# Kernel optimization log

Measured on AMD Instinct MI355X. Metric: run time of the kernel, lower is better.

## Reference

```python
import jax, jax.numpy as jnp
import numpy as np

B, S, D = 2, 2048, 1024
H, DH = 16, 64
E, K, FH = 8, 2, 4096
AUX_W = 0.01
EPS = 1e-6


def setup_inputs() -> dict:
    key = jax.random.key(0)
    ks = jax.random.split(key, 20)
    init = lambda k, shape: (jax.random.normal(k, shape, dtype=jnp.float32) * 0.02)
    return {
        'x': jax.random.normal(ks[0], (B, S, D), dtype=jnp.float32),
        'ln1_s': jnp.ones((D,), jnp.float32), 'ln1_b': jnp.zeros((D,), jnp.float32),
        'Wq': init(ks[1], (D, H * DH)), 'bq': jnp.zeros((H * DH,), jnp.float32),
        'Wk': init(ks[2], (D, H * DH)), 'bk': jnp.zeros((H * DH,), jnp.float32),
        'Wv': init(ks[3], (D, H * DH)), 'bv': jnp.zeros((H * DH,), jnp.float32),
        'Wo': init(ks[4], (H * DH, D)), 'bo': jnp.zeros((D,), jnp.float32),
        'ln2_s': jnp.ones((D,), jnp.float32), 'ln2_b': jnp.zeros((D,), jnp.float32),
        'Wg': init(ks[5], (D, E)), 'bg': jnp.zeros((E,), jnp.float32),
        'W1': init(ks[6], (E, D, FH)), 'b1': jnp.zeros((E, FH), jnp.float32),
        'W2': init(ks[7], (E, FH, D)), 'b2': jnp.zeros((E, D), jnp.float32),
    }


def _layer_norm(x, scale, bias):
    mu = jnp.mean(x, axis=-1, keepdims=True)
    var = jnp.mean(jnp.square(x - mu), axis=-1, keepdims=True)
    return (x - mu) * jax.lax.rsqrt(var + EPS) * scale + bias


def _causal_attn(x, Wq, bq, Wk, bk, Wv, bv, Wo, bo):
    b, s, _ = x.shape
    q = (x @ Wq + bq).reshape(b, s, H, DH)
    k = (x @ Wk + bk).reshape(b, s, H, DH)
    v = (x @ Wv + bv).reshape(b, s, H, DH)
    scores = jnp.einsum('bqhd,bkhd->bhqk', q, k) / jnp.sqrt(jnp.float32(DH))
    causal = jnp.tril(jnp.ones((s, s), dtype=bool))
    scores = jnp.where(causal, scores, jnp.finfo(scores.dtype).min)
    attn = jax.nn.softmax(scores, axis=-1)
    out = jnp.einsum('bhqk,bkhd->bqhd', attn, v).reshape(b, s, H * DH)
    return out @ Wo + bo


def _moe(x, Wg, bg, W1, b1, W2, b2):
    # x: (B,S,D) -> tokens (T,D)
    T = x.shape[0] * x.shape[1]
    xf = x.reshape(T, D)
    logits = xf @ Wg + bg                      # (T,E)
    probs = jax.nn.softmax(logits, axis=-1)
    topv, topi = jax.lax.top_k(probs, K)       # (T,K)
    topv = topv / jnp.sum(topv, axis=-1, keepdims=True)
    combine = jnp.zeros((T, E), xf.dtype).at[jnp.arange(T)[:, None], topi].set(topv)
    out = jnp.zeros((T, D), xf.dtype)
    for e in range(E):  # fixed small expert loop
        h = jax.nn.gelu(xf @ W1[e] + b1[e])
        out = out + combine[:, e:e + 1] * (h @ W2[e] + b2[e])
    # load-balance aux loss
    frac = jnp.mean((combine > 0).astype(jnp.float32), axis=0)
    pmean = jnp.mean(probs, axis=0)
    aux = AUX_W * E * jnp.sum(frac * pmean)
    return out.reshape(x.shape), aux


def reference(x, ln1_s, ln1_b, Wq, bq, Wk, bk, Wv, bv, Wo, bo,
              ln2_s, ln2_b, Wg, bg, W1, b1, W2, b2):
    working = x
    attn_in = _layer_norm(working, ln1_s, ln1_b)
    attn_out = _causal_attn(attn_in, Wq, bq, Wk, bk, Wv, bv, Wo, bo)
    working = working + attn_out
    ffn_in = _layer_norm(working, ln2_s, ln2_b)
    ffn_out, aux = _moe(ffn_in, Wg, bg, W1, b1, W2, b2)
    output = working + ffn_out
    return output, aux
```

## Files before the change

kernel.cpp:

```cpp
#include <hip/hip_runtime.h>
#include <hip/hip_bf16.h>
#include <math.h>

#define Bb 2
#define Ss 2048
#define Dd 1024
#define Hh 16
#define DH 64
#define Ee 8
#define FH 4096
#define Tt (Bb*Ss)

typedef __attribute__((ext_vector_type(8))) short short8;
typedef __attribute__((ext_vector_type(4))) short short4v;
typedef __attribute__((ext_vector_type(4))) float float4v;

static __device__ inline short f2bf(float f) {
    __hip_bfloat16 h = __float2bfloat16(f);
    return *reinterpret_cast<short*>(&h);
}

static __device__ inline void glds16(const __hip_bfloat16* g, __hip_bfloat16* l) {
    __builtin_amdgcn_global_load_lds(
        (const __attribute__((address_space(1))) unsigned int*)g,
        (__attribute__((address_space(3))) unsigned int*)l, 16, 0, 0);
}

__global__ __launch_bounds__(256) void ln_kernel(const float* __restrict__ x,
                                                 const float* __restrict__ sc,
                                                 const float* __restrict__ bi,
                                                 __hip_bfloat16* __restrict__ y) {
    int t = blockIdx.x, tid = threadIdx.x;
    const float* xr = x + (size_t)t * Dd;
    float s1 = 0.f, s2 = 0.f;
    for (int d = tid; d < Dd; d += 256) { float v = xr[d]; s1 += v; s2 += v * v; }
    __shared__ float r1[256], r2[256];
    r1[tid] = s1; r2[tid] = s2; __syncthreads();
    for (int off = 128; off > 0; off >>= 1) {
        if (tid < off) { r1[tid] += r1[tid + off]; r2[tid] += r2[tid + off]; }
        __syncthreads();
    }
    float mu = r1[0] * (1.f / Dd);
    float var = r2[0] * (1.f / Dd) - mu * mu;
    float rstd = rsqrtf(var + 1e-6f);
    __hip_bfloat16* yr = y + (size_t)t * Dd;
    for (int d = tid; d < Dd; d += 256) {
        float v = xr[d];
        yr[d] = __float2bfloat16((v - mu) * rstd * sc[d] + bi[d]);
    }
}

__global__ __launch_bounds__(256) void transpose_qkvo(
    const float* W0, const float* W1, const float* W2, const float* W3,
    __hip_bfloat16* T0, __hip_bfloat16* T1, __hip_bfloat16* T2, __hip_bfloat16* T3) {
    int z = blockIdx.z;
    const float* W = (z == 0) ? W0 : (z == 1) ? W1 : (z == 2) ? W2 : W3;
    __hip_bfloat16* Wt = (z == 0) ? T0 : (z == 1) ? T1 : (z == 2) ? T2 : T3;
    __shared__ float tile[64][65];
    int k0 = blockIdx.y * 64, n0 = blockIdx.x * 64;
    int tx = threadIdx.x & 15, ty = threadIdx.x >> 4;
    #pragma unroll
    for (int p = 0; p < 4; p++) {
        float4 v = *(const float4*)(&W[(size_t)(k0 + ty + p * 16) * Dd + n0 + tx * 4]);
        tile[ty + p * 16][tx * 4 + 0] = v.x;
        tile[ty + p * 16][tx * 4 + 1] = v.y;
        tile[ty + p * 16][tx * 4 + 2] = v.z;
        tile[ty + p * 16][tx * 4 + 3] = v.w;
    }
    __syncthreads();
    #pragma unroll
    for (int p = 0; p < 4; p++) {
        int n = ty + p * 16;
        short4v pk;
        pk[0] = f2bf(tile[tx * 4 + 0][n]);
        pk[1] = f2bf(tile[tx * 4 + 1][n]);
        pk[2] = f2bf(tile[tx * 4 + 2][n]);
        pk[3] = f2bf(tile[tx * 4 + 3][n]);
        *(short4v*)(&Wt[(size_t)(n0 + n) * Dd + k0 + tx * 4]) = pk;
    }
}

__global__ __launch_bounds__(256) void transpose_we(const float* __restrict__ W,
                                                    __hip_bfloat16* __restrict__ Wt,
                                                    int Kd, int N) {
    int e = blockIdx.z;
    W  += (size_t)e * Kd * N;
    Wt += (size_t)e * Kd * N;
    __shared__ float tile[64][65];
    int k0 = blockIdx.y * 64, n0 = blockIdx.x * 64;
    int tx = threadIdx.x & 15, ty = threadIdx.x >> 4;
    #pragma unroll
    for (int p = 0; p < 4; p++) {
        float4 v = *(const float4*)(&W[(size_t)(k0 + ty + p * 16) * N + n0 + tx * 4]);
        tile[ty + p * 16][tx * 4 + 0] = v.x;
        tile[ty + p * 16][tx * 4 + 1] = v.y;
        tile[ty + p * 16][tx * 4 + 2] = v.z;
        tile[ty + p * 16][tx * 4 + 3] = v.w;
    }
    __syncthreads();
    #pragma unroll
    for (int p = 0; p < 4; p++) {
        int n = ty + p * 16;
        short4v pk;
        pk[0] = f2bf(tile[tx * 4 + 0][n]);
        pk[1] = f2bf(tile[tx * 4 + 1][n]);
        pk[2] = f2bf(tile[tx * 4 + 2][n]);
        pk[3] = f2bf(tile[tx * 4 + 3][n]);
        *(short4v*)(&Wt[(size_t)(n0 + n) * Kd + k0 + tx * 4]) = pk;
    }
}

template<int MODE, int NS = 1>
__global__ __launch_bounds__(256) void gemm_mfma(
    const __hip_bfloat16* __restrict__ A, const __hip_bfloat16* __restrict__ Bt,
    const float* __restrict__ bias, void* __restrict__ Cv,
    int M, int N, int Kd,
    const int* __restrict__ bucket, const int* __restrict__ cnts,
    const int* __restrict__ bases, const float* __restrict__ residual,
    const float* __restrict__ bias_k, const float* __restrict__ bias_v,
    void* __restrict__ Ck, void* __restrict__ Cv2)
{
    int Me = M;
    const int* rowIdx = nullptr;
    int hbase = 0;
    int ksplit = 0;
    int zsel = 0;
    if (MODE == 2 || MODE == 3) {
        int e = (NS == 2) ? (blockIdx.z >> 1) : blockIdx.z;
        if (NS == 2) ksplit = blockIdx.z & 1;
        Me = cnts[e];
        hbase = bases[e];
        Bt += (size_t)e * N * Kd;
        bias += (size_t)e * N;
        if (MODE == 2) rowIdx = bucket + e * Tt;
        if (MODE == 3) A += (size_t)hbase * Kd;
    }
    if (MODE == 5) {
        zsel = blockIdx.z;
        Bt += (size_t)zsel * Dd * Dd;
        if (zsel == 1) bias = bias_k;
        if (zsel == 2) bias = bias_v;
    }
    int m0 = blockIdx.y * 128;
    if (m0 >= Me) return;
    int n0 = blockIdx.x * 128;

    __shared__ __hip_bfloat16 As[2 * 128 * 32];
    __shared__ __hip_bfloat16 Bs[2 * 128 * 32];

    int tid = threadIdx.x;
    int lane = tid & 63, wave = tid >> 6;
    int wm = (wave & 1) * 64, wn = (wave >> 1) * 64;
    int quad = lane >> 4, l16 = lane & 15;

    int rs = lane >> 2;
    int sslot = (lane & 3) ^ ((lane >> 3) & 3);
    int rowS0 = 16 * (2 * wave + 0) + rs;
    int rowS1 = 16 * (2 * wave + 1) + rs;

    const __hip_bfloat16 *gA0, *gA1;
    if (MODE == 2) {
        int g0 = m0 + rowS0, g1 = m0 + rowS1;
        int r0 = (g0 < Me) ? rowIdx[g0] : 0;
        int r1 = (g1 < Me) ? rowIdx[g1] : 0;
        gA0 = A + (size_t)r0 * Kd + sslot * 8;
        gA1 = A + (size_t)r1 * Kd + sslot * 8;
    } else {
        gA0 = A + (size_t)(m0 + rowS0) * Kd + sslot * 8;
        gA1 = A + (size_t)(m0 + rowS1) * Kd + sslot * 8;
    }
    const __hip_bfloat16* gB0 = Bt + (size_t)(n0 + rowS0) * Kd + sslot * 8;
    const __hip_bfloat16* gB1 = Bt + (size_t)(n0 + rowS1) * Kd + sslot * 8;

    __hip_bfloat16* lA0 = As + (2 * wave + 0) * 512;
    __hip_bfloat16* lA1 = As + (2 * wave + 1) * 512;
    __hip_bfloat16* lB0 = Bs + (2 * wave + 0) * 512;
    __hip_bfloat16* lB1 = Bs + (2 * wave + 1) * 512;

    int rsw = (l16 >> 1) & 3;
    int rdoff = (quad ^ rsw) * 8;

    float4v acc[4][4];
    #pragma unroll
    for (int i = 0; i < 4; i++)
        #pragma unroll
        for (int j = 0; j < 4; j++) acc[i][j] = (float4v)0.f;

    const int NT = Kd >> 5;
    int t0s = 0, t1s = NT;
    if (NS == 2) { int hlf = NT >> 1; t0s = ksplit * hlf; t1s = t0s + hlf; }

    {
        int ko = t0s << 5;
        glds16(gA0 + ko, lA0);
        glds16(gA1 + ko, lA1);
        glds16(gB0 + ko, lB0);
        glds16(gB1 + ko, lB1);
    }
    __syncthreads();

    int cur = 0;
    for (int t = t0s; t < t1s; t++) {
        if (t + 1 < t1s) {
            int ko = (t + 1) << 5;
            int bo = (cur ^ 1) * 4096;
            glds16(gA0 + ko, lA0 + bo);
            glds16(gA1 + ko, lA1 + bo);
            glds16(gB0 + ko, lB0 + bo);
            glds16(gB1 + ko, lB1 + bo);
        }
        int cb = cur * 4096;
        short8 af[4], bf[4];
        #pragma unroll
        for (int i = 0; i < 4; i++)
            af[i] = *(const short8*)(&As[cb + (wm + i * 16 + l16) * 32 + rdoff]);
        #pragma unroll
        for (int j = 0; j < 4; j++)
            bf[j] = *(const short8*)(&Bs[cb + (wn + j * 16 + l16) * 32 + rdoff]);
        #pragma unroll
        for (int i = 0; i < 4; i++)
            #pragma unroll
            for (int j = 0; j < 4; j++)
                acc[i][j] = __builtin_amdgcn_mfma_f32_16x16x32_bf16(af[i], bf[j], acc[i][j], 0, 0, 0);
        __syncthreads();
        cur ^= 1;
    }

    #pragma unroll
    for (int i = 0; i < 4; i++) {
        #pragma unroll
        for (int j = 0; j < 4; j++) {
            int col = n0 + wn + j * 16 + l16;
            float bsv = (MODE == 3 && NS == 2 && ksplit == 1) ? 0.f : bias[col];
            if (MODE == 4 || (MODE == 5 && zsel == 2)) {
                __hip_bfloat16* vt = (__hip_bfloat16*)((MODE == 5) ? Cv2 : Cv);
                int mb = m0 + wm + i * 16 + quad * 4;
                int b = mb >> 11, s0 = mb & (Ss - 1);
                int h = col >> 6, d = col & (DH - 1);
                short4v pk;
                #pragma unroll
                for (int r = 0; r < 4; r++) pk[r] = f2bf(acc[i][j][r] + bsv);
                *(short4v*)(vt + ((size_t)(b * Hh + h) * DH + d) * Ss + s0) = pk;
                continue;
            }
            #pragma unroll
            for (int r = 0; r < 4; r++) {
                int m = m0 + wm + i * 16 + quad * 4 + r;
                if (m >= Me) continue;
                float val = acc[i][j][r] + bsv;
                if (MODE == 0) {
                    ((__hip_bfloat16*)Cv)[(size_t)m * N + col] = __float2bfloat16(val);
                } else if (MODE == 5) {
                    __hip_bfloat16* co = (__hip_bfloat16*)((zsel == 0) ? Cv : Ck);
                    co[(size_t)m * N + col] = __float2bfloat16(val);
                } else if (MODE == 1) {
                    ((float*)Cv)[(size_t)m * N + col] = val + residual[(size_t)m * N + col];
                } else if (MODE == 2) {
                    float z = 0.7978845608028654f * (val + 0.044715f * val * val * val);
                    float eg = __expf(2.f * z);
                    float th = 1.f - __fdividef(2.f, eg + 1.f);
                    ((__hip_bfloat16*)Cv)[(size_t)(hbase + m) * N + col] =
                        __float2bfloat16(0.5f * val * (1.f + th));
                } else {
                    float* o3 = (float*)((NS == 2 && ksplit == 1) ? Cv2 : Cv);
                    o3[(size_t)(hbase + m) * N + col] = val;
                }
            }
        }
    }
}

__global__ __launch_bounds__(256) void attn_mfma(const __hip_bfloat16* __restrict__ q,
                                                 const __hip_bfloat16* __restrict__ k,
                                                 const __hip_bfloat16* __restrict__ Vt,
                                                 __hip_bfloat16* __restrict__ out) {
    int h = blockIdx.x, tile = blockIdx.y, b = blockIdx.z;
    int wave = threadIdx.x >> 6, lane = threadIdx.x & 63;
    int quad = lane >> 4, l16 = lane & 15;
    int q0 = tile * 64 + wave * 16;
    int tb = b * Ss;

    __shared__ __hip_bfloat16 Ks[32 * 72];
    __shared__ __hip_bfloat16 Vs[64 * 40];

    const __hip_bfloat16* qp = q + (size_t)(tb + q0 + l16) * (Hh * DH) + h * DH + quad * 8;
    short8 qf0 = *(const short8*)(qp);
    short8 qf1 = *(const short8*)(qp + 32);

    float4v oc[4];
    #pragma unroll
    for (int i = 0; i < 4; i++) oc[i] = (float4v)0.f;
    float lsum = 0.f;

    const __hip_bfloat16* kbase = k + (size_t)tb * (Hh * DH) + h * DH;
    const __hip_bfloat16* vbase = Vt + ((size_t)(b * Hh + h) * DH) * Ss;
    int qglob = q0 + l16;
    int srcA = (quad & 1) * 32 + l16;
    int srcB = srcA + 16;
    int sel = quad >> 1;
    int nsteps = 2 * tile + 2;

    int krow = threadIdx.x >> 3, kg = threadIdx.x & 7;
    int vd   = threadIdx.x >> 2, vg = threadIdx.x & 3;

    short8 kv = *(const short8*)(kbase + (size_t)krow * (Hh * DH) + kg * 8);
    short8 vv = *(const short8*)(vbase + (size_t)vd * Ss + vg * 8);

    for (int st = 0; st < nsteps; st++) {
        int k0 = st * 32;
        *(short8*)(&Ks[krow * 72 + kg * 8]) = kv;
        *(short8*)(&Vs[vd * 40 + vg * 8]) = vv;
        __syncthreads();
        if (st + 1 < nsteps) {
            kv = *(const short8*)(kbase + (size_t)(k0 + 32 + krow) * (Hh * DH) + kg * 8);
            vv = *(const short8*)(vbase + (size_t)vd * Ss + (k0 + 32) + vg * 8);
        }

        short8 a0 = *(const short8*)(&Ks[l16 * 72 + quad * 8]);
        short8 a1 = *(const short8*)(&Ks[l16 * 72 + 32 + quad * 8]);
        short8 a2 = *(const short8*)(&Ks[(l16 + 16) * 72 + quad * 8]);
        short8 a3 = *(const short8*)(&Ks[(l16 + 16) * 72 + 32 + quad * 8]);

        float4v c0 = (float4v)0.f, c1 = (float4v)0.f;
        c0 = __builtin_amdgcn_mfma_f32_16x16x32_bf16(a0, qf0, c0, 0, 0, 0);
        c0 = __builtin_amdgcn_mfma_f32_16x16x32_bf16(a1, qf1, c0, 0, 0, 0);
        c1 = __builtin_amdgcn_mfma_f32_16x16x32_bf16(a2, qf0, c1, 0, 0, 0);
        c1 = __builtin_amdgcn_mfma_f32_16x16x32_bf16(a3, qf1, c1, 0, 0, 0);

        float p0[4], p1[4];
        #pragma unroll
        for (int r = 0; r < 4; r++) {
            int key0 = k0 + quad * 4 + r;
            int key1 = key0 + 16;
            p0[r] = (key0 <= qglob) ? __expf(c0[r] * 0.125f - 4.f) : 0.f;
            p1[r] = (key1 <= qglob) ? __expf(c1[r] * 0.125f - 4.f) : 0.f;
            lsum += p0[r] + p1[r];
        }

        short8 pf;
        #pragma unroll
        for (int r = 0; r < 4; r++) {
            float t0 = __shfl(p0[r], srcA), t1 = __shfl(p1[r], srcA);
            pf[r] = f2bf(sel ? t1 : t0);
            float u0 = __shfl(p0[r], srcB), u1 = __shfl(p1[r], srcB);
            pf[4 + r] = f2bf(sel ? u1 : u0);
        }

        #pragma unroll
        for (int nt = 0; nt < 4; nt++) {
            short8 bv = *(const short8*)(&Vs[(nt * 16 + l16) * 40 + quad * 8]);
            oc[nt] = __builtin_amdgcn_mfma_f32_16x16x32_bf16(pf, bv, oc[nt], 0, 0, 0);
        }
        __syncthreads();
    }

    lsum += __shfl_xor(lsum, 16);
    lsum += __shfl_xor(lsum, 32);
    float linv[4];
    #pragma unroll
    for (int r = 0; r < 4; r++) linv[r] = 1.f / __shfl(lsum, quad * 4 + r);

    #pragma unroll
    for (int nt = 0; nt < 4; nt++) {
        #pragma unroll
        for (int r = 0; r < 4; r++) {
            int tokq = tb + q0 + quad * 4 + r;
            out[(size_t)tokq * (Hh * DH) + h * DH + nt * 16 + l16] =
                __float2bfloat16(oc[nt][r] * linv[r]);
        }
    }
}

#define GT 64
__global__ __launch_bounds__(256) void gate_kernel(const float* __restrict__ wk,
                                                   const float* __restrict__ g2s,
                                                   const float* __restrict__ g2b,
                                                   const float* __restrict__ Wg,
                                                   const float* __restrict__ bg,
                                                   float* __restrict__ psum,
                                                   int* __restrict__ counts,
                                                   int* __restrict__ bucket,
                                                   int* __restrict__ eidx,
                                                   int* __restrict__ epos,
                                                   float* __restrict__ ew) {
    int t0 = blockIdx.x * GT;
    int wave = threadIdx.x >> 6, lane = threadIdx.x & 63;

    __shared__ float sp[GT][Ee];
    __shared__ int   sel_e[2][GT];
    __shared__ int   spos[2][GT];
    __shared__ int   lbase[Ee];

    for (int i = wave; i < GT; i += 4) {
        int t = t0 + i;
        const float* xr = wk + (size_t)t * Dd;
        float xv[16];
        float s1 = 0.f, sq = 0.f;
        #pragma unroll
        for (int j = 0; j < 16; j++) {
            float v = xr[lane + j * 64];
            xv[j] = v; s1 += v; sq += v * v;
        }
        #pragma unroll
        for (int off = 32; off; off >>= 1) { s1 += __shfl_xor(s1, off); sq += __shfl_xor(sq, off); }
        float mu = s1 * (1.f / Dd), var = sq * (1.f / Dd) - mu * mu;
        float rstd = rsqrtf(var + 1e-6f);
        float acc[Ee] = {};
        #pragma unroll
        for (int j = 0; j < 16; j++) {
            int d = lane + j * 64;
            float xn = (xv[j] - mu) * rstd * g2s[d] + g2b[d];
            const float* wr = Wg + d * Ee;
            #pragma unroll
            for (int e = 0; e < Ee; e++) acc[e] += xn * wr[e];
        }
        #pragma unroll
        for (int e = 0; e < Ee; e++)
            #pragma unroll
            for (int off = 32; off; off >>= 1) acc[e] += __shfl_xor(acc[e], off);
        if (lane == 0) {
            float lg[Ee], mx = -1e30f;
            #pragma unroll
            for (int e = 0; e < Ee; e++) { lg[e] = acc[e] + bg[e]; mx = fmaxf(mx, lg[e]); }
            float p[Ee], ssum = 0.f;
            #pragma unroll
            for (int e = 0; e < Ee; e++) { p[e] = __expf(lg[e] - mx); ssum += p[e]; }
            float ise = 1.f / ssum;
            #pragma unroll
            for (int e = 0; e < Ee; e++) { p[e] *= ise; sp[i][e] = p[e]; }
            int e1 = 0;
            for (int e = 1; e < Ee; e++) if (p[e] > p[e1]) e1 = e;
            int e2 = -1;
            for (int e = 0; e < Ee; e++) if (e != e1 && (e2 < 0 || p[e] > p[e2])) e2 = e;
            sel_e[0][i] = e1; sel_e[1][i] = e2;
            float w1 = p[e1], w2 = p[e2], isw = 1.f / (w1 + w2);
            eidx[2 * t] = e1; ew[2 * t] = w1 * isw;
            eidx[2 * t + 1] = e2; ew[2 * t + 1] = w2 * isw;
        }
    }
    __syncthreads();

    if (threadIdx.x < Ee) {
        int e = threadIdx.x;
        int local = 0;
        for (int i = 0; i < GT; i++) {
            if (sel_e[0][i] == e) spos[0][i] = local++;
            if (sel_e[1][i] == e) spos[1][i] = local++;
        }
        lbase[e] = atomicAdd(&counts[e], local);
        float ps = 0.f;
        for (int i = 0; i < GT; i++) ps += sp[i][e];
        atomicAdd(&psum[e], ps);
    }
    __syncthreads();

    if (threadIdx.x < GT) {
        int i = threadIdx.x, t = t0 + i;
        #pragma unroll
        for (int s = 0; s < 2; s++) {
            int e = sel_e[s][i];
            int pos = lbase[e] + spos[s][i];
            bucket[e * Tt + pos] = t;
            epos[2 * t + s] = pos;
        }
    }
}

__global__ void zero_init(float* psum, int* counts) {
    int i = threadIdx.x;
    if (i < Ee) { psum[i] = 0.f; counts[i] = 0; }
}

__global__ void prefix_kernel(const int* counts, int* bases) {
    if (threadIdx.x == 0) {
        int run = 0;
        for (int e = 0; e < Ee; e++) { bases[e] = run; run += counts[e]; }
    }
}

__global__ __launch_bounds__(256) void combine_out(const float* __restrict__ working,
                                                   const float* __restrict__ O2,
                                                   const float* __restrict__ O2b,
                                                   const int* __restrict__ bases,
                                                   const int* __restrict__ eidx,
                                                   const int* __restrict__ epos,
                                                   const float* __restrict__ ew,
                                                   float* __restrict__ out,
                                                   int ns) {
    int t = blockIdx.x, tid = threadIdx.x;
    int e0 = eidx[2 * t], e1 = eidx[2 * t + 1];
    size_t r0 = (size_t)(bases[e0] + epos[2 * t]) * Dd;
    size_t r1 = (size_t)(bases[e1] + epos[2 * t + 1]) * Dd;
    float w0 = ew[2 * t], w1 = ew[2 * t + 1];
    const float4* wr = (const float4*)(working + (size_t)t * Dd);
    const float4* o0 = (const float4*)(O2 + r0);
    const float4* o1 = (const float4*)(O2 + r1);
    float4 a = wr[tid], x0 = o0[tid], x1 = o1[tid];
    if (ns == 2) {
        const float4* p0 = (const float4*)(O2b + r0);
        const float4* p1 = (const float4*)(O2b + r1);
        float4 y0 = p0[tid], y1 = p1[tid];
        x0.x += y0.x; x0.y += y0.y; x0.z += y0.z; x0.w += y0.w;
        x1.x += y1.x; x1.y += y1.y; x1.z += y1.z; x1.w += y1.w;
    }
    float4* dst = (float4*)(out + (size_t)t * Dd);
    dst[tid] = make_float4(a.x + w0 * x0.x + w1 * x1.x,
                           a.y + w0 * x0.y + w1 * x1.y,
                           a.z + w0 * x0.z + w1 * x1.z,
                           a.w + w0 * x0.w + w1 * x1.w);
}

__global__ void aux_kernel(const int* counts, const float* psum, float* out) {
    if (threadIdx.x == 0 && blockIdx.x == 0) {
        float a = 0.f;
        for (int e = 0; e < Ee; e++)
            a += (counts[e] * (1.f / Tt)) * (psum[e] * (1.f / Tt));
        out[0] = 0.01f * (float)Ee * a;
    }
}

extern "C" void kernel_launch(void* const* d_in, const int* in_sizes, int n_in,
                              void* d_out, int out_size, void* d_ws, size_t ws_size,
                              hipStream_t stream) {
    const float* x     = (const float*)d_in[0];
    const float* ln1_s = (const float*)d_in[1];
    const float* ln1_b = (const float*)d_in[2];
    const float* Wq    = (const float*)d_in[3];
    const float* bq    = (const float*)d_in[4];
    const float* Wk    = (const float*)d_in[5];
    const float* bk    = (const float*)d_in[6];
    const float* Wv    = (const float*)d_in[7];
    const float* bv    = (const float*)d_in[8];
    const float* Wo    = (const float*)d_in[9];
    const float* bo    = (const float*)d_in[10];
    const float* ln2_s = (const float*)d_in[11];
    const float* ln2_b = (const float*)d_in[12];
    const float* Wg    = (const float*)d_in[13];
    const float* bg    = (const float*)d_in[14];
    const float* W1    = (const float*)d_in[15];
    const float* b1    = (const float*)d_in[16];
    const float* W2    = (const float*)d_in[17];
    const float* b2    = (const float*)d_in[18];

    const size_t MBy = 1u << 20;
    char* base = (char*)d_ws;
    __hip_bfloat16* attn_in = (__hip_bfloat16*)(base);
    __hip_bfloat16* qbf     = (__hip_bfloat16*)(base + 8 * MBy);
    __hip_bfloat16* kbf     = (__hip_bfloat16*)(base + 16 * MBy);
    __hip_bfloat16* Vt      = (__hip_bfloat16*)(base + 24 * MBy);
    float*          working = (float*)(base + 32 * MBy);
    __hip_bfloat16* ffn_in  = (__hip_bfloat16*)(base + 48 * MBy);
    __hip_bfloat16* Hbuf    = (__hip_bfloat16*)(base + 56 * MBy);
    float*          O2      = (float*)(base);
    __hip_bfloat16* WT      = (__hip_bfloat16*)(base + 120 * MBy);
    __hip_bfloat16* WqT     = (__hip_bfloat16*)(base + 120 * MBy);
    __hip_bfloat16* WkT     = (__hip_bfloat16*)(base + 122 * MBy);
    __hip_bfloat16* WvT     = (__hip_bfloat16*)(base + 124 * MBy);
    __hip_bfloat16* WoT     = (__hip_bfloat16*)(base + 126 * MBy);
    char* rt = base + 184 * MBy;
    int*   bucket = (int*)rt;
    int*   counts = (int*)(rt + Ee * Tt * 4);
    int*   bases  = counts + 64;
    float* psum   = (float*)(bases + 64);
    int*   eidx   = (int*)(psum + 64);
    int*   epos   = eidx + 2 * Tt;
    float* ew     = (float*)(epos + 2 * Tt);

    bool   sk  = (ws_size >= (size_t)224 * MBy);
    float* O2b = sk ? (float*)(base + 192 * MBy) : O2;

    float* out  = (float*)d_out;
    float* auxp = out + (size_t)Tt * Dd;

    zero_init<<<1, 64, 0, stream>>>(psum, counts);
    transpose_qkvo<<<dim3(Dd / 64, Dd / 64, 4), 256, 0, stream>>>(
        Wq, Wk, Wv, Wo, WqT, WkT, WvT, WoT);
    ln_kernel<<<Tt, 256, 0, stream>>>(x, ln1_s, ln1_b, attn_in);

    dim3 gqkv(Dd / 128, Tt / 128);
    gemm_mfma<5><<<dim3(Dd / 128, Tt / 128, 3), 256, 0, stream>>>(
        attn_in, WqT, bq, qbf, Tt, Dd, Dd,
        nullptr, nullptr, nullptr, nullptr, bk, bv, kbf, Vt);

    attn_mfma<<<dim3(Hh, Ss / 64, Bb), 256, 0, stream>>>(qbf, kbf, Vt, attn_in);

    gemm_mfma<1><<<gqkv, 256, 0, stream>>>(attn_in, WoT, bo, working, Tt, Dd, Dd,
                                           nullptr, nullptr, nullptr, x,
                                           nullptr, nullptr, nullptr, nullptr);

    ln_kernel<<<Tt, 256, 0, stream>>>(working, ln2_s, ln2_b, ffn_in);
    gate_kernel<<<Tt / GT, 256, 0, stream>>>(working, ln2_s, ln2_b, Wg, bg,
                                             psum, counts, bucket, eidx, epos, ew);
    prefix_kernel<<<1, 64, 0, stream>>>(counts, bases);

    transpose_we<<<dim3(FH / 64, Dd / 64, Ee), 256, 0, stream>>>(W1, WT, Dd, FH);
    gemm_mfma<2><<<dim3(FH / 128, Tt / 128, Ee), 256, 0, stream>>>(
        ffn_in, WT, b1, Hbuf, Tt, FH, Dd, bucket, counts, bases, nullptr,
        nullptr, nullptr, nullptr, nullptr);
    transpose_we<<<dim3(Dd / 64, FH / 64, Ee), 256, 0, stream>>>(W2, WT, FH, Dd);
    if (sk) {
        gemm_mfma<3, 2><<<dim3(Dd / 128, Tt / 128, 2 * Ee), 256, 0, stream>>>(
            Hbuf, WT, b2, O2, Tt, Dd, FH, bucket, counts, bases, nullptr,
            nullptr, nullptr, nullptr, O2b);
    } else {
        gemm_mfma<3, 1><<<dim3(Dd / 128, Tt / 128, Ee), 256, 0, stream>>>(
            Hbuf, WT, b2, O2, Tt, Dd, FH, bucket, counts, bases, nullptr,
            nullptr, nullptr, nullptr, nullptr);
    }

    combine_out<<<Tt, 256, 0, stream>>>(working, O2, O2b, bases, eidx, epos, ew, out,
                                        sk ? 2 : 1);
    aux_kernel<<<1, 64, 0, stream>>>(counts, psum, auxp);
}
```

Measured before the change: 842.3 us.

## Add dedicated 256x256-tile MoE up-projection GEMM with fused GELU

Replaces the generic 128x128 gemm_mfma<2> launch for the expert W1 GEMM with a specialised kernel that uses 256x256 tiles, 512 threads and 8 waves. Each wave holds an 8x4 grid of MFMA accumulators, loads are double-buffered and issued straight to LDS, and the LDS reads are swizzled. The larger tile is meant to raise arithmetic intensity and cut redundant global loads of the gathered token rows and the weights. In exchange, register pressure is high (128 accumulator floats per thread), and more work is wasted on partially filled 256-row tiles at the end of each expert bucket.

```diff
diff --git a/kernel.cpp b/kernel.cpp
--- a/kernel.cpp
+++ b/kernel.cpp
@@ -270,6 +270,112 @@
     }
 }
 
+__global__ __launch_bounds__(512, 2) void gemm_moe1(
+    const __hip_bfloat16* __restrict__ A, const __hip_bfloat16* __restrict__ Bt,
+    const float* __restrict__ bias, __hip_bfloat16* __restrict__ H,
+    const int* __restrict__ bucket, const int* __restrict__ cnts,
+    const int* __restrict__ bases)
+{
+    int e = blockIdx.z;
+    int Me = cnts[e];
+    int hbase = bases[e];
+    Bt += (size_t)e * FH * Dd;
+    bias += (size_t)e * FH;
+    const int* rowIdx = bucket + e * Tt;
+    int m0 = blockIdx.y * 256;
+    if (m0 >= Me) return;
+    int n0 = blockIdx.x * 256;
+
+    __shared__ __hip_bfloat16 As[2 * 256 * 32];
+    __shared__ __hip_bfloat16 Bs[2 * 256 * 32];
+
+    int tid = threadIdx.x;
+    int lane = tid & 63, wave = tid >> 6;
+    int wr = wave >> 2, wc = wave & 3;
+    int quad = lane >> 4, l16 = lane & 15;
+
+    int rs = lane >> 2;
+    int sslot = (lane & 3) ^ ((lane >> 3) & 3);
+    int rowS0 = 16 * wave + rs;
+    int rowS1 = 128 + 16 * wave + rs;
+
+    int g0 = m0 + rowS0, g1 = m0 + rowS1;
+    int r0 = (g0 < Me) ? rowIdx[g0] : 0;
+    int r1 = (g1 < Me) ? rowIdx[g1] : 0;
+    const __hip_bfloat16* gA0 = A + (size_t)r0 * Dd + sslot * 8;
+    const __hip_bfloat16* gA1 = A + (size_t)r1 * Dd + sslot * 8;
+    const __hip_bfloat16* gB0 = Bt + (size_t)(n0 + rowS0) * Dd + sslot * 8;
+    const __hip_bfloat16* gB1 = Bt + (size_t)(n0 + rowS1) * Dd + sslot * 8;
+
+    __hip_bfloat16* lA0 = As + (size_t)wave * 512;
+    __hip_bfloat16* lA1 = As + (size_t)(8 + wave) * 512;
+    __hip_bfloat16* lB0 = Bs + (size_t)wave * 512;
+    __hip_bfloat16* lB1 = Bs + (size_t)(8 + wave) * 512;
+
+    int rsw = (l16 >> 1) & 3;
+    int rdoff = (quad ^ rsw) * 8;
+
+    float4v acc[8][4];
+    #pragma unroll
+    for (int i = 0; i < 8; i++)
+        #pragma unroll
+        for (int j = 0; j < 4; j++) acc[i][j] = (float4v)0.f;
+
+    glds16(gA0, lA0);
+    glds16(gA1, lA1);
+    glds16(gB0, lB0);
+    glds16(gB1, lB1);
+    __syncthreads();
+
+    const int NT = Dd >> 5;
+    int cur = 0;
+    for (int t = 0; t < NT; t++) {
+        if (t + 1 < NT) {
+            int ko = (t + 1) << 5;
+            int bo = (cur ^ 1) * 8192;
+            glds16(gA0 + ko, lA0 + bo);
+            glds16(gA1 + ko, lA1 + bo);
+            glds16(gB0 + ko, lB0 + bo);
+            glds16(gB1 + ko, lB1 + bo);
+        }
+        int cb = cur * 8192;
+        short8 af[8], bf[4];
+        #pragma unroll
+        for (int i = 0; i < 8; i++)
+            af[i] = *(const short8*)(&As[cb + (wr * 128 + i * 16 + l16) * 32 + rdoff]);
+        #pragma unroll
+        for (int j = 0; j < 4; j++)
+            bf[j] = *(const short8*)(&Bs[cb + (wc * 64 + j * 16 + l16) * 32 + rdoff]);
+        #pragma unroll
+        for (int i = 0; i < 8; i++)
+            #pragma unroll
+            for (int j = 0; j < 4; j++)
+                acc[i][j] = __builtin_amdgcn_mfma_f32_16x16x32_bf16(af[i], bf[j], acc[i][j], 0, 0, 0);
+        __syncthreads();
+        cur ^= 1;
+    }
+
+    #pragma unroll
+    for (int i = 0; i < 8; i++) {
+        #pragma unroll
+        for (int j = 0; j < 4; j++) {
+            int col = n0 + wc * 64 + j * 16 + l16;
+            float bsv = bias[col];
+            #pragma unroll
+            for (int r = 0; r < 4; r++) {
+                int m = m0 + wr * 128 + i * 16 + quad * 4 + r;
+                if (m >= Me) continue;
+                float val = acc[i][j][r] + bsv;
+                float z = 0.7978845608028654f * (val + 0.044715f * val * val * val);
+                float eg = __expf(2.f * z);
+                float th = 1.f - __fdividef(2.f, eg + 1.f);
+                H[(size_t)(hbase + m) * FH + col] =
+                    __float2bfloat16(0.5f * val * (1.f + th));
+            }
+        }
+    }
+}
+
 __global__ __launch_bounds__(256) void attn_mfma(const __hip_bfloat16* __restrict__ q,
                                                  const __hip_bfloat16* __restrict__ k,
                                                  const __hip_bfloat16* __restrict__ Vt,
@@ -594,9 +700,8 @@
     prefix_kernel<<<1, 64, 0, stream>>>(counts, bases);
 
     transpose_we<<<dim3(FH / 64, Dd / 64, Ee), 256, 0, stream>>>(W1, WT, Dd, FH);
-    gemm_mfma<2><<<dim3(FH / 128, Tt / 128, Ee), 256, 0, stream>>>(
-        ffn_in, WT, b1, Hbuf, Tt, FH, Dd, bucket, counts, bases, nullptr,
-        nullptr, nullptr, nullptr, nullptr);
+    gemm_moe1<<<dim3(FH / 256, Tt / 256, Ee), 512, 0, stream>>>(
+        ffn_in, WT, b1, Hbuf, bucket, counts, bases);
     transpose_we<<<dim3(Dd / 64, FH / 64, Ee), 256, 0, stream>>>(W2, WT, FH, Dd);
     if (sk) {
         gemm_mfma<3, 2><<<dim3(Dd / 128, Tt / 128, 2 * Ee), 256, 0, stream>>>(
```

Measured after the change: 906.9 us. +7.7%, slower.
